# Kernel optimization log

Hardware: AMD Instinct MI355X
Metric: run time of the kernel (lower is better)

Reference implementation:

```python
import jax, jax.numpy as jnp
import numpy as np

N_NODES, N_EDGES, D_IN, D_HID, D_OUT = 100000, 3200000, 128, 64, 10


def _gcn_norm(src, dst, n):
    # symmetric normalization deg^{-1/2}[src] * deg^{-1/2}[dst]; edge weights = 1
    ones = jnp.ones(src.shape[0], jnp.float32)
    deg = jax.ops.segment_sum(ones, dst, num_segments=n)
    dinv = jnp.where(deg > 0, jax.lax.rsqrt(jnp.maximum(deg, 1.0)), 0.0)
    return dinv[src] * dinv[dst]


def _gcn_conv(x, W, b, src, dst, norm, n):
    h = x @ W                                   # [N, out]
    msg = norm[:, None] * jnp.take(h, src, axis=0)  # [E+N, out]
    return jax.ops.segment_sum(msg, dst, num_segments=n) + b


def setup_inputs() -> dict:
    key = jax.random.key(0)
    ks = jax.random.split(key, 8)
    x = jax.random.normal(ks[0], (N_NODES, D_IN), jnp.float32)
    edge_index = jax.random.randint(ks[1], (2, N_EDGES), 0, N_NODES, jnp.int32)
    def glorot(k, fan_in, fan_out):
        s = (6.0 / (fan_in + fan_out)) ** 0.5
        return jax.random.uniform(k, (fan_in, fan_out), jnp.float32, -s, s)
    return {
        "x": x,
        "edge_index": edge_index,
        "W1": glorot(ks[2], D_IN, D_HID), "b1": jnp.zeros((D_HID,), jnp.float32),
        "W2": glorot(ks[3], D_HID, D_HID), "b2": jnp.zeros((D_HID,), jnp.float32),
        "W3": glorot(ks[4], D_HID, D_OUT), "b3": jnp.zeros((D_OUT,), jnp.float32),
    }


def reference(x, edge_index, W1, b1, W2, b2, W3, b3):
    n = x.shape[0]
    loops = jnp.arange(n, dtype=edge_index.dtype)
    src = jnp.concatenate([edge_index[0], loops])  # add self-loops (PyG default)
    dst = jnp.concatenate([edge_index[1], loops])
    norm = _gcn_norm(src, dst, n)                  # identical for all 3 layers
    h = jax.nn.relu(_gcn_conv(x, W1, b1, src, dst, norm, n))
    h = jax.nn.relu(_gcn_conv(h, W2, b2, src, dst, norm, n))
    return _gcn_conv(h, W3, b3, src, dst, norm, n)
```

## Files before the change

### kernel.cpp

```cpp
#include <hip/hip_runtime.h>


constexpr int BK_SHIFT = 6;
constexpr int BK_NODES = 64;
constexpr int BK_CAP   = 2432;
constexpr int MAXNB    = 1568;

typedef __attribute__((ext_vector_type(8))) short short8_t;
typedef __attribute__((ext_vector_type(4))) float f32x4_t;

__device__ __forceinline__ unsigned short f2bf(float f) {
    unsigned u = __builtin_bit_cast(unsigned, f);
    u += 0x7FFF + ((u >> 16) & 1);
    return (unsigned short)(u >> 16);
}
__device__ __forceinline__ unsigned pack2(float lo, float hi) {
    return (unsigned)f2bf(lo) | ((unsigned)f2bf(hi) << 16);
}
__device__ __forceinline__ float bf_lo(unsigned d) {
    return __builtin_bit_cast(float, d << 16);
}
__device__ __forceinline__ float bf_hi(unsigned d) {
    return __builtin_bit_cast(float, d & 0xFFFF0000u);
}
__device__ __forceinline__ float bf1(unsigned short u) {
    return __builtin_bit_cast(float, (unsigned)u << 16);
}

__global__ void k_partition(const int* __restrict__ src, const int* __restrict__ dst,
                            int E, int nb, int* __restrict__ cursor,
                            unsigned* __restrict__ inter) {
    __shared__ int lcount[MAXNB];
    __shared__ int gbase[MAXNB];
    int t = threadIdx.x;
    int base = blockIdx.x * 16384;
    for (int i = t; i < MAXNB; i += 512) lcount[i] = 0;
    __syncthreads();
    int sv[32], dvv[32];
#pragma unroll
    for (int j = 0; j < 32; j++) {
        int idx = base + j * 512 + t;
        if (idx < E) {
            sv[j] = src[idx]; dvv[j] = dst[idx];
            atomicAdd(&lcount[dvv[j] >> BK_SHIFT], 1);
        } else dvv[j] = -1;
    }
    __syncthreads();
    for (int i = t; i < nb; i += 512) {
        int c = lcount[i]; int g = 0;
        if (c) g = atomicAdd(&cursor[i], c);
        gbase[i] = g; lcount[i] = 0;
    }
    __syncthreads();
#pragma unroll
    for (int j = 0; j < 32; j++) {
        if (dvv[j] >= 0) {
            int b = dvv[j] >> BK_SHIFT;
            int r = gbase[b] + atomicAdd(&lcount[b], 1);
            if (r < BK_CAP)
                inter[(size_t)b * BK_CAP + r] =
                    (unsigned)sv[j] | ((unsigned)(dvv[j] & (BK_NODES - 1)) << 20);
        }
    }
}

__global__ void k_dinvb(const unsigned* __restrict__ inter, const int* __restrict__ cursor,
                        float* __restrict__ dinv, int N) {
    __shared__ int hist[BK_NODES];
    int t = threadIdx.x, b = blockIdx.x;
    if (t < BK_NODES) hist[t] = 0;
    __syncthreads();
    int cnt = min(cursor[b], BK_CAP);
    const unsigned* ip = inter + (size_t)b * BK_CAP;
    for (int i = t; i < cnt; i += 256) atomicAdd(&hist[ip[i] >> 20], 1);
    __syncthreads();
    if (t < BK_NODES) {
        int d = b * BK_NODES + t;
        if (d < N) dinv[d] = rsqrtf((float)(hist[t] + 1));
    }
}

template <int K, bool IN_F32>
__global__ __launch_bounds__(256) void k_gemmMF(const void* __restrict__ Xv,
                           const float* __restrict__ W,
                           const float* __restrict__ dinv,
                           unsigned short* __restrict__ Y, int n) {
    constexpr int KP = K + 8;
    __shared__ unsigned short Al[64 * KP];
    __shared__ unsigned short Bl[64 * KP];
    int t = threadIdx.x;
    int nb = blockIdx.x * 64;
    if (IN_F32) {
        const float* X = (const float*)Xv;
        for (int i = t * 4; i < 64 * K; i += 1024) {
            int r = i / K, c = i % K;
            int node = nb + r;
            float4 v = {0.f, 0.f, 0.f, 0.f};
            if (node < n) v = *reinterpret_cast<const float4*>(X + (size_t)node * K + c);
            uint2 pk = {pack2(v.x, v.y), pack2(v.z, v.w)};
            *reinterpret_cast<uint2*>(&Al[r * KP + c]) = pk;
        }
    } else {
        const unsigned short* X = (const unsigned short*)Xv;
        for (int i = t * 4; i < 64 * K; i += 1024) {
            int r = i / K, c = i % K;
            int node = nb + r;
            uint2 pk = {0u, 0u};
            if (node < n) pk = *reinterpret_cast<const uint2*>(X + (size_t)node * K + c);
            *reinterpret_cast<uint2*>(&Al[r * KP + c]) = pk;
        }
    }
    {
        int c = t & 63, kb = t >> 6;
        for (int k = kb; k < K; k += 4)
            Bl[c * KP + k] = f2bf(W[k * 64 + c]);
    }
    __syncthreads();
    int w = t >> 6, lane = t & 63;
    int ml = lane & 15, kg = lane >> 4;
    f32x4_t acc[4] = {{0,0,0,0},{0,0,0,0},{0,0,0,0},{0,0,0,0}};
    for (int ks = 0; ks < K / 32; ks++) {
        int ko = ks * 32 + kg * 8;
        short8_t a = *reinterpret_cast<const short8_t*>(&Al[(16 * w + ml) * KP + ko]);
#pragma unroll
        for (int c = 0; c < 4; c++) {
            short8_t b = *reinterpret_cast<const short8_t*>(&Bl[(16 * c + ml) * KP + ko]);
            acc[c] = __builtin_amdgcn_mfma_f32_16x16x32_bf16(a, b, acc[c], 0, 0, 0);
        }
    }
#pragma unroll
    for (int r = 0; r < 4; r++) {
        int grow = nb + 16 * w + kg * 4 + r;
        if (grow < n) {
            float dv = dinv[grow];
#pragma unroll
            for (int c = 0; c < 4; c++)
                Y[(size_t)grow * 64 + 16 * c + ml] = f2bf(dv * acc[c][r]);
        }
    }
}

__global__ void k_gemm10(const float* __restrict__ X, const float* __restrict__ W,
                         const float* __restrict__ dinv, unsigned short* __restrict__ Y, int n) {
    __shared__ float ws[64 * 10];
    __shared__ float xs[16 * 64];
    int t = threadIdx.x;
    for (int i = t; i < 640; i += 256) ws[i] = W[i];
    int nb = blockIdx.x * 16;
    for (int i = t; i < 16 * 64; i += 256) {
        int r = i >> 6, c = i & 63;
        int node = nb + r;
        xs[i] = (node < n) ? X[(size_t)node * 64 + c] : 0.f;
    }
    __syncthreads();
    int ns = t >> 4, c = t & 15;
    if (c < 10) {
        float acc = 0.f;
        for (int k = 0; k < 64; k++) acc += xs[ns * 64 + k] * ws[k * 10 + c];
        int node = nb + ns;
        if (node < n) Y[(size_t)node * 10 + c] = f2bf(dinv[node] * acc);
    }
}

template <int OBF>
__global__ __launch_bounds__(512) void k_agg64(const unsigned short* __restrict__ H,
                        const unsigned* __restrict__ inter, const int* __restrict__ cursor,
                        const float* __restrict__ bias, void* __restrict__ outv,
                        int N, int relu) {
    __shared__ unsigned raw[BK_CAP];
    __shared__ unsigned srt[BK_CAP];
    __shared__ int hist[BK_NODES];
    __shared__ int offs[BK_NODES + 1];
    __shared__ int cur[BK_NODES];
    int t = threadIdx.x, b = blockIdx.x;
    if (t < BK_NODES) hist[t] = 0;
    __syncthreads();
    int cnt = min(cursor[b], BK_CAP);
    const unsigned* ip = inter + (size_t)b * BK_CAP;
    for (int i = t; i < cnt; i += 512) {
        unsigned r = ip[i];
        raw[i] = r;
        atomicAdd(&hist[r >> 20], 1);
    }
    __syncthreads();
    if (t < BK_NODES) {
        int v = hist[t];
        int inc = v;
#pragma unroll
        for (int d = 1; d < 64; d <<= 1) {
            int o = __shfl_up(inc, d);
            if (t >= d) inc += o;
        }
        offs[t + 1] = inc;
        if (t == 0) offs[0] = 0;
        cur[t] = inc - v;
    }
    __syncthreads();
    for (int i = t; i < cnt; i += 512) {
        unsigned r = raw[i];
        int pos = atomicAdd(&cur[r >> 20], 1);
        srt[pos] = r & 0xFFFFFu;
    }
    __syncthreads();
    int wv = t >> 6, lane = t & 63;
    int esub = lane >> 3, cg = lane & 7;
    const unsigned short* Hc = H + (cg << 3);
    for (int nd = wv; nd < BK_NODES; nd += 8) {
        int d = b * BK_NODES + nd;
        if (d >= N) break;
        int o0 = offs[nd], o1 = offs[nd + 1];
        float a0 = 0.f, a1 = 0.f, a2 = 0.f, a3 = 0.f;
        float a4 = 0.f, a5 = 0.f, a6 = 0.f, a7 = 0.f;
        int e = o0 + esub;
        for (; e + 8 < o1; e += 16) {
            int s0 = srt[e], s1 = srt[e + 8];
            const uint4 v0 = *reinterpret_cast<const uint4*>(Hc + ((size_t)s0 << 6));
            const uint4 v1 = *reinterpret_cast<const uint4*>(Hc + ((size_t)s1 << 6));
            a0 += bf_lo(v0.x); a1 += bf_hi(v0.x); a2 += bf_lo(v0.y); a3 += bf_hi(v0.y);
            a4 += bf_lo(v0.z); a5 += bf_hi(v0.z); a6 += bf_lo(v0.w); a7 += bf_hi(v0.w);
            a0 += bf_lo(v1.x); a1 += bf_hi(v1.x); a2 += bf_lo(v1.y); a3 += bf_hi(v1.y);
            a4 += bf_lo(v1.z); a5 += bf_hi(v1.z); a6 += bf_lo(v1.w); a7 += bf_hi(v1.w);
        }
        for (; e < o1; e += 8) {
            int s0 = srt[e];
            const uint4 v0 = *reinterpret_cast<const uint4*>(Hc + ((size_t)s0 << 6));
            a0 += bf_lo(v0.x); a1 += bf_hi(v0.x); a2 += bf_lo(v0.y); a3 += bf_hi(v0.y);
            a4 += bf_lo(v0.z); a5 += bf_hi(v0.z); a6 += bf_lo(v0.w); a7 += bf_hi(v0.w);
        }
#pragma unroll
        for (int m = 8; m <= 32; m <<= 1) {
            a0 += __shfl_xor(a0, m); a1 += __shfl_xor(a1, m);
            a2 += __shfl_xor(a2, m); a3 += __shfl_xor(a3, m);
            a4 += __shfl_xor(a4, m); a5 += __shfl_xor(a5, m);
            a6 += __shfl_xor(a6, m); a7 += __shfl_xor(a7, m);
        }
        if (esub == 0) {
            float dv = rsqrtf((float)(hist[nd] + 1));
            const uint4 sv = *reinterpret_cast<const uint4*>(Hc + ((size_t)d << 6));
            float s[8] = {bf_lo(sv.x), bf_hi(sv.x), bf_lo(sv.y), bf_hi(sv.y),
                          bf_lo(sv.z), bf_hi(sv.z), bf_lo(sv.w), bf_hi(sv.w)};
            float acc[8] = {a0, a1, a2, a3, a4, a5, a6, a7};
            const float* bp = bias + cg * 8;
            float o[8];
#pragma unroll
            for (int j = 0; j < 8; j++) {
                float val = dv * (acc[j] + s[j]) + bp[j];
                if (relu) val = fmaxf(val, 0.f);
                o[j] = val;
            }
            if (OBF) {
                unsigned short* op = (unsigned short*)outv + (size_t)d * 64 + cg * 8;
                uint4 pk = {pack2(o[0], o[1]), pack2(o[2], o[3]),
                            pack2(o[4], o[5]), pack2(o[6], o[7])};
                *reinterpret_cast<uint4*>(op) = pk;
            } else {
                float* op = (float*)outv + (size_t)d * 64 + cg * 8;
                float4 r0 = {o[0], o[1], o[2], o[3]}, r1 = {o[4], o[5], o[6], o[7]};
                *reinterpret_cast<float4*>(op)     = r0;
                *reinterpret_cast<float4*>(op + 4) = r1;
            }
        }
    }
}

__global__ __launch_bounds__(512) void k_agg10(const unsigned short* __restrict__ H,
                        const unsigned* __restrict__ inter, const int* __restrict__ cursor,
                        const float* __restrict__ b3, float* __restrict__ out, int N) {
    __shared__ unsigned raw[BK_CAP];
    __shared__ unsigned srt[BK_CAP];
    __shared__ int hist[BK_NODES];
    __shared__ int offs[BK_NODES + 1];
    __shared__ int cur[BK_NODES];
    int t = threadIdx.x, b = blockIdx.x;
    if (t < BK_NODES) hist[t] = 0;
    __syncthreads();
    int cnt = min(cursor[b], BK_CAP);
    const unsigned* ip = inter + (size_t)b * BK_CAP;
    for (int i = t; i < cnt; i += 512) {
        unsigned r = ip[i];
        raw[i] = r;
        atomicAdd(&hist[r >> 20], 1);
    }
    __syncthreads();
    if (t < BK_NODES) {
        int v = hist[t];
        int inc = v;
#pragma unroll
        for (int d = 1; d < 64; d <<= 1) {
            int o = __shfl_up(inc, d);
            if (t >= d) inc += o;
        }
        offs[t + 1] = inc;
        if (t == 0) offs[0] = 0;
        cur[t] = inc - v;
    }
    __syncthreads();
    for (int i = t; i < cnt; i += 512) {
        unsigned r = raw[i];
        int pos = atomicAdd(&cur[r >> 20], 1);
        srt[pos] = r & 0xFFFFFu;
    }
    __syncthreads();
    int wv = t >> 6, lane = t & 63;
    int esub = lane >> 4, c = lane & 15;
    for (int nd = wv; nd < BK_NODES; nd += 8) {
        int d = b * BK_NODES + nd;
        if (d >= N) break;
        int o0 = offs[nd], o1 = offs[nd + 1];
        float acc = 0.f;
        if (c < 10) {
            int e = o0 + esub;
            for (; e + 4 < o1; e += 8) {
                int s0 = srt[e], s1 = srt[e + 4];
                acc += bf1(H[(size_t)s0 * 10 + c]) + bf1(H[(size_t)s1 * 10 + c]);
            }
            if (e < o1) acc += bf1(H[(size_t)srt[e] * 10 + c]);
        }
        acc += __shfl_xor(acc, 16);
        acc += __shfl_xor(acc, 32);
        if (esub == 0 && c < 10) {
            float dv = rsqrtf((float)(hist[nd] + 1));
            out[(size_t)d * 10 + c] = dv * (acc + bf1(H[(size_t)d * 10 + c])) + b3[c];
        }
    }
}

extern "C" void kernel_launch(void* const* d_in, const int* in_sizes, int n_in,
                              void* d_out, int out_size, void* d_ws, size_t ws_size,
                              hipStream_t stream) {
    const float* x  = (const float*)d_in[0];
    const int*   ei = (const int*)d_in[1];
    const float* W1 = (const float*)d_in[2];
    const float* b1 = (const float*)d_in[3];
    const float* W2 = (const float*)d_in[4];
    const float* b2 = (const float*)d_in[5];
    const float* W3 = (const float*)d_in[6];
    const float* b3 = (const float*)d_in[7];

    int N = in_sizes[0] / 128;
    int E = in_sizes[1] / 2;
    const int* esrc = ei;
    const int* edst = ei + E;
    int nb = (N + BK_NODES - 1) >> BK_SHIFT;

    char* p = (char*)d_ws;
    auto carve = [&](size_t bytes) -> void* {
        void* r = p;
        p += (bytes + 255) & ~(size_t)255;
        return r;
    };
    int*      cursor = (int*)carve((size_t)MAXNB * 4);
    unsigned* inter  = (unsigned*)carve((size_t)nb * BK_CAP * 4);
    float*    dinv   = (float*)carve((size_t)N * 4);
    unsigned short* Hs = (unsigned short*)carve((size_t)N * 64 * 2);
    unsigned short* Gb = (unsigned short*)carve((size_t)N * 64 * 2);
    float*    Gf     = (float*)carve((size_t)N * 64 * 4);
    unsigned short* Hs10 = (unsigned short*)carve((size_t)N * 10 * 2);
    (void)ws_size; (void)n_in; (void)out_size;

    hipMemsetAsync(cursor, 0, (size_t)nb * 4, stream);
    k_partition<<<(E + 16383) / 16384, 512, 0, stream>>>(esrc, edst, E, nb, cursor, inter);
    k_dinvb<<<nb, 256, 0, stream>>>(inter, cursor, dinv, N);

    k_gemmMF<128, true><<<(N + 63) / 64, 256, 0, stream>>>(x, W1, dinv, Hs, N);
    k_agg64<1><<<nb, 512, 0, stream>>>(Hs, inter, cursor, b1, Gb, N, 1);
    k_gemmMF<64, false><<<(N + 63) / 64, 256, 0, stream>>>(Gb, W2, dinv, Hs, N);
    k_agg64<0><<<nb, 512, 0, stream>>>(Hs, inter, cursor, b2, Gf, N, 1);
    k_gemm10<<<(N + 15) / 16, 256, 0, stream>>>(Gf, W3, dinv, Hs10, N);
    k_agg10<<<nb, 512, 0, stream>>>(Hs10, inter, cursor, b3, (float*)d_out, N);
}
```

Baseline: 246.0 us.

## Presort bucket edges once and split 64-wide aggregation into feature quarters

```diff
diff --git a/kernel.cpp b/kernel.cpp
--- a/kernel.cpp
+++ b/kernel.cpp
@@ -64,20 +64,50 @@
     }
 }
 
-__global__ void k_dinvb(const unsigned* __restrict__ inter, const int* __restrict__ cursor,
+__global__ __launch_bounds__(512) void k_sort(const unsigned* __restrict__ inter,
+                        const int* __restrict__ cursor,
+                        unsigned* __restrict__ srt_g, int* __restrict__ offs_g,
                         float* __restrict__ dinv, int N) {
+    __shared__ unsigned raw[BK_CAP];
+    __shared__ unsigned srt[BK_CAP];
     __shared__ int hist[BK_NODES];
+    __shared__ int offs[BK_NODES + 1];
+    __shared__ int cur[BK_NODES];
     int t = threadIdx.x, b = blockIdx.x;
     if (t < BK_NODES) hist[t] = 0;
     __syncthreads();
     int cnt = min(cursor[b], BK_CAP);
     const unsigned* ip = inter + (size_t)b * BK_CAP;
-    for (int i = t; i < cnt; i += 256) atomicAdd(&hist[ip[i] >> 20], 1);
+    for (int i = t; i < cnt; i += 512) {
+        unsigned r = ip[i];
+        raw[i] = r;
+        atomicAdd(&hist[r >> 20], 1);
+    }
     __syncthreads();
     if (t < BK_NODES) {
+        int v = hist[t];
+        int inc = v;
+#pragma unroll
+        for (int d = 1; d < 64; d <<= 1) {
+            int o = __shfl_up(inc, d);
+            if (t >= d) inc += o;
+        }
+        offs[t + 1] = inc;
+        if (t == 0) offs[0] = 0;
+        cur[t] = inc - v;
         int d = b * BK_NODES + t;
         if (d < N) dinv[d] = rsqrtf((float)(hist[t] + 1));
     }
+    __syncthreads();
+    for (int i = t; i < cnt; i += 512) {
+        unsigned r = raw[i];
+        int pos = atomicAdd(&cur[r >> 20], 1);
+        srt[pos] = r & 0xFFFFFu;
+    }
+    __syncthreads();
+    unsigned* sg = srt_g + (size_t)b * BK_CAP;
+    for (int i = t; i < cnt; i += 512) sg[i] = srt[i];
+    if (t < BK_NODES + 1) offs_g[b * (BK_NODES + 1) + t] = offs[t];
 }
 
 template <int K, bool IN_F32>
@@ -135,7 +165,7 @@
             float dv = dinv[grow];
 #pragma unroll
             for (int c = 0; c < 4; c++)
-                Y[(size_t)grow * 64 + 16 * c + ml] = f2bf(dv * acc[c][r]);
+                Y[((size_t)c * n + grow) * 16 + ml] = f2bf(dv * acc[c][r]);
         }
     }
 }
@@ -163,153 +193,97 @@
 }
 
 template <int OBF>
-__global__ __launch_bounds__(512) void k_agg64(const unsigned short* __restrict__ H,
-                        const unsigned* __restrict__ inter, const int* __restrict__ cursor,
-                        const float* __restrict__ bias, void* __restrict__ outv,
-                        int N, int relu) {
-    __shared__ unsigned raw[BK_CAP];
+__global__ __launch_bounds__(256) void k_agg64s(const unsigned short* __restrict__ Hs,
+                        const unsigned* __restrict__ srt_g, const int* __restrict__ offs_g,
+                        const float* __restrict__ dinv, const float* __restrict__ bias,
+                        void* __restrict__ outv, int N, int nb, int relu) {
     __shared__ unsigned srt[BK_CAP];
-    __shared__ int hist[BK_NODES];
     __shared__ int offs[BK_NODES + 1];
-    __shared__ int cur[BK_NODES];
-    int t = threadIdx.x, b = blockIdx.x;
-    if (t < BK_NODES) hist[t] = 0;
-    __syncthreads();
-    int cnt = min(cursor[b], BK_CAP);
-    const unsigned* ip = inter + (size_t)b * BK_CAP;
-    for (int i = t; i < cnt; i += 512) {
-        unsigned r = ip[i];
-        raw[i] = r;
-        atomicAdd(&hist[r >> 20], 1);
-    }
-    __syncthreads();
-    if (t < BK_NODES) {
-        int v = hist[t];
-        int inc = v;
-#pragma unroll
-        for (int d = 1; d < 64; d <<= 1) {
-            int o = __shfl_up(inc, d);
-            if (t >= d) inc += o;
-        }
-        offs[t + 1] = inc;
-        if (t == 0) offs[0] = 0;
-        cur[t] = inc - v;
-    }
-    __syncthreads();
-    for (int i = t; i < cnt; i += 512) {
-        unsigned r = raw[i];
-        int pos = atomicAdd(&cur[r >> 20], 1);
-        srt[pos] = r & 0xFFFFFu;
-    }
-    __syncthreads();
+    int t = threadIdx.x;
+    int x = blockIdx.x & 7;
+    int q = x >> 1;
+    int b = (blockIdx.x >> 3) * 2 + (x & 1);
+    if (b >= nb) return;
+    if (t < BK_NODES + 1) offs[t] = offs_g[b * (BK_NODES + 1) + t];
+    __syncthreads();
+    int cnt = offs[BK_NODES];
+    const unsigned* sg = srt_g + (size_t)b * BK_CAP;
+    for (int i = t; i < cnt; i += 256) srt[i] = sg[i];
+    __syncthreads();
+    const unsigned short* Hq = Hs + (size_t)q * N * 16;
+    const float* bq = bias + q * 16;
     int wv = t >> 6, lane = t & 63;
-    int esub = lane >> 3, cg = lane & 7;
-    const unsigned short* Hc = H + (cg << 3);
-    for (int nd = wv; nd < BK_NODES; nd += 8) {
+    int es = lane >> 2, cg = lane & 3;
+    for (int nd = wv; nd < BK_NODES; nd += 4) {
         int d = b * BK_NODES + nd;
         if (d >= N) break;
         int o0 = offs[nd], o1 = offs[nd + 1];
         float a0 = 0.f, a1 = 0.f, a2 = 0.f, a3 = 0.f;
-        float a4 = 0.f, a5 = 0.f, a6 = 0.f, a7 = 0.f;
-        int e = o0 + esub;
-        for (; e + 8 < o1; e += 16) {
-            int s0 = srt[e], s1 = srt[e + 8];
-            const uint4 v0 = *reinterpret_cast<const uint4*>(Hc + ((size_t)s0 << 6));
-            const uint4 v1 = *reinterpret_cast<const uint4*>(Hc + ((size_t)s1 << 6));
-            a0 += bf_lo(v0.x); a1 += bf_hi(v0.x); a2 += bf_lo(v0.y); a3 += bf_hi(v0.y);
-            a4 += bf_lo(v0.z); a5 += bf_hi(v0.z); a6 += bf_lo(v0.w); a7 += bf_hi(v0.w);
-            a0 += bf_lo(v1.x); a1 += bf_hi(v1.x); a2 += bf_lo(v1.y); a3 += bf_hi(v1.y);
-            a4 += bf_lo(v1.z); a5 += bf_hi(v1.z); a6 += bf_lo(v1.w); a7 += bf_hi(v1.w);
-        }
-        for (; e < o1; e += 8) {
+        int e = o0 + es;
+        for (; e + 16 < o1; e += 32) {
+            int s0 = srt[e], s1 = srt[e + 16];
+            const uint2 v0 = *reinterpret_cast<const uint2*>(Hq + (size_t)s0 * 16 + cg * 4);
+            const uint2 v1 = *reinterpret_cast<const uint2*>(Hq + (size_t)s1 * 16 + cg * 4);
+            a0 += bf_lo(v0.x) + bf_lo(v1.x); a1 += bf_hi(v0.x) + bf_hi(v1.x);
+            a2 += bf_lo(v0.y) + bf_lo(v1.y); a3 += bf_hi(v0.y) + bf_hi(v1.y);
+        }
+        for (; e < o1; e += 16) {
             int s0 = srt[e];
-            const uint4 v0 = *reinterpret_cast<const uint4*>(Hc + ((size_t)s0 << 6));
-            a0 += bf_lo(v0.x); a1 += bf_hi(v0.x); a2 += bf_lo(v0.y); a3 += bf_hi(v0.y);
-            a4 += bf_lo(v0.z); a5 += bf_hi(v0.z); a6 += bf_lo(v0.w); a7 += bf_hi(v0.w);
-        }
-#pragma unroll
-        for (int m = 8; m <= 32; m <<= 1) {
+            const uint2 v0 = *reinterpret_cast<const uint2*>(Hq + (size_t)s0 * 16 + cg * 4);
+            a0 += bf_lo(v0.x); a1 += bf_hi(v0.x);
+            a2 += bf_lo(v0.y); a3 += bf_hi(v0.y);
+        }
+#pragma unroll
+        for (int m = 4; m <= 32; m <<= 1) {
             a0 += __shfl_xor(a0, m); a1 += __shfl_xor(a1, m);
             a2 += __shfl_xor(a2, m); a3 += __shfl_xor(a3, m);
-            a4 += __shfl_xor(a4, m); a5 += __shfl_xor(a5, m);
-            a6 += __shfl_xor(a6, m); a7 += __shfl_xor(a7, m);
-        }
-        if (esub == 0) {
-            float dv = rsqrtf((float)(hist[nd] + 1));
-            const uint4 sv = *reinterpret_cast<const uint4*>(Hc + ((size_t)d << 6));
-            float s[8] = {bf_lo(sv.x), bf_hi(sv.x), bf_lo(sv.y), bf_hi(sv.y),
-                          bf_lo(sv.z), bf_hi(sv.z), bf_lo(sv.w), bf_hi(sv.w)};
-            float acc[8] = {a0, a1, a2, a3, a4, a5, a6, a7};
-            const float* bp = bias + cg * 8;
-            float o[8];
-#pragma unroll
-            for (int j = 0; j < 8; j++) {
-                float val = dv * (acc[j] + s[j]) + bp[j];
+        }
+        if (es == 0) {
+            float dv = dinv[d];
+            const uint2 sv = *reinterpret_cast<const uint2*>(Hq + (size_t)d * 16 + cg * 4);
+            float o[4] = {bf_lo(sv.x), bf_hi(sv.x), bf_lo(sv.y), bf_hi(sv.y)};
+            float ac[4] = {a0, a1, a2, a3};
+#pragma unroll
+            for (int j = 0; j < 4; j++) {
+                float val = dv * (ac[j] + o[j]) + bq[cg * 4 + j];
                 if (relu) val = fmaxf(val, 0.f);
                 o[j] = val;
             }
             if (OBF) {
-                unsigned short* op = (unsigned short*)outv + (size_t)d * 64 + cg * 8;
-                uint4 pk = {pack2(o[0], o[1]), pack2(o[2], o[3]),
-                            pack2(o[4], o[5]), pack2(o[6], o[7])};
-                *reinterpret_cast<uint4*>(op) = pk;
+                unsigned short* op = (unsigned short*)outv + (size_t)d * 64 + q * 16 + cg * 4;
+                uint2 pk = {pack2(o[0], o[1]), pack2(o[2], o[3])};
+                *reinterpret_cast<uint2*>(op) = pk;
             } else {
-                float* op = (float*)outv + (size_t)d * 64 + cg * 8;
-                float4 r0 = {o[0], o[1], o[2], o[3]}, r1 = {o[4], o[5], o[6], o[7]};
-                *reinterpret_cast<float4*>(op)     = r0;
-                *reinterpret_cast<float4*>(op + 4) = r1;
+                float* op = (float*)outv + (size_t)d * 64 + q * 16 + cg * 4;
+                float4 r0 = {o[0], o[1], o[2], o[3]};
+                *reinterpret_cast<float4*>(op) = r0;
             }
         }
     }
 }
 
-__global__ __launch_bounds__(512) void k_agg10(const unsigned short* __restrict__ H,
-                        const unsigned* __restrict__ inter, const int* __restrict__ cursor,
-                        const float* __restrict__ b3, float* __restrict__ out, int N) {
-    __shared__ unsigned raw[BK_CAP];
+__global__ __launch_bounds__(512) void k_agg10s(const unsigned short* __restrict__ H,
+                        const unsigned* __restrict__ srt_g, const int* __restrict__ offs_g,
+                        const float* __restrict__ dinv, const float* __restrict__ b3,
+                        float* __restrict__ out, int N) {
     __shared__ unsigned srt[BK_CAP];
-    __shared__ int hist[BK_NODES];
     __shared__ int offs[BK_NODES + 1];
-    __shared__ int cur[BK_NODES];
     int t = threadIdx.x, b = blockIdx.x;
-    if (t < BK_NODES) hist[t] = 0;
-    __syncthreads();
-    int cnt = min(cursor[b], BK_CAP);
-    const unsigned* ip = inter + (size_t)b * BK_CAP;
-    for (int i = t; i < cnt; i += 512) {
-        unsigned r = ip[i];
-        raw[i] = r;
-        atomicAdd(&hist[r >> 20], 1);
-    }
-    __syncthreads();
-    if (t < BK_NODES) {
-        int v = hist[t];
-        int inc = v;
-#pragma unroll
-        for (int d = 1; d < 64; d <<= 1) {
-            int o = __shfl_up(inc, d);
-            if (t >= d) inc += o;
-        }
-        offs[t + 1] = inc;
-        if (t == 0) offs[0] = 0;
-        cur[t] = inc - v;
-    }
-    __syncthreads();
-    for (int i = t; i < cnt; i += 512) {
-        unsigned r = raw[i];
-        int pos = atomicAdd(&cur[r >> 20], 1);
-        srt[pos] = r & 0xFFFFFu;
-    }
+    if (t < BK_NODES + 1) offs[t] = offs_g[b * (BK_NODES + 1) + t];
+    __syncthreads();
+    int cnt = offs[BK_NODES];
+    const unsigned* sg = srt_g + (size_t)b * BK_CAP;
+    for (int i = t; i < cnt; i += 512) srt[i] = sg[i];
     __syncthreads();
     int wv = t >> 6, lane = t & 63;
-    int esub = lane >> 4, c = lane & 15;
+    int es = lane >> 4, c = lane & 15;
     for (int nd = wv; nd < BK_NODES; nd += 8) {
         int d = b * BK_NODES + nd;
         if (d >= N) break;
         int o0 = offs[nd], o1 = offs[nd + 1];
         float acc = 0.f;
         if (c < 10) {
-            int e = o0 + esub;
+            int e = o0 + es;
             for (; e + 4 < o1; e += 8) {
                 int s0 = srt[e], s1 = srt[e + 4];
                 acc += bf1(H[(size_t)s0 * 10 + c]) + bf1(H[(size_t)s1 * 10 + c]);
@@ -318,8 +292,8 @@
         }
         acc += __shfl_xor(acc, 16);
         acc += __shfl_xor(acc, 32);
-        if (esub == 0 && c < 10) {
-            float dv = rsqrtf((float)(hist[nd] + 1));
+        if (es == 0 && c < 10) {
+            float dv = dinv[d];
             out[(size_t)d * 10 + c] = dv * (acc + bf1(H[(size_t)d * 10 + c])) + b3[c];
         }
     }
@@ -351,6 +325,8 @@
     };
     int*      cursor = (int*)carve((size_t)MAXNB * 4);
     unsigned* inter  = (unsigned*)carve((size_t)nb * BK_CAP * 4);
+    unsigned* srt_g  = (unsigned*)carve((size_t)nb * BK_CAP * 4);
+    int*      offs_g = (int*)carve((size_t)nb * (BK_NODES + 1) * 4);
     float*    dinv   = (float*)carve((size_t)N * 4);
     unsigned short* Hs = (unsigned short*)carve((size_t)N * 64 * 2);
     unsigned short* Gb = (unsigned short*)carve((size_t)N * 64 * 2);
@@ -358,14 +334,16 @@
     unsigned short* Hs10 = (unsigned short*)carve((size_t)N * 10 * 2);
     (void)ws_size; (void)n_in; (void)out_size;
 
+    int gridA = ((nb + 1) / 2) * 8;
+
     hipMemsetAsync(cursor, 0, (size_t)nb * 4, stream);
     k_partition<<<(E + 16383) / 16384, 512, 0, stream>>>(esrc, edst, E, nb, cursor, inter);
-    k_dinvb<<<nb, 256, 0, stream>>>(inter, cursor, dinv, N);
+    k_sort<<<nb, 512, 0, stream>>>(inter, cursor, srt_g, offs_g, dinv, N);
 
     k_gemmMF<128, true><<<(N + 63) / 64, 256, 0, stream>>>(x, W1, dinv, Hs, N);
-    k_agg64<1><<<nb, 512, 0, stream>>>(Hs, inter, cursor, b1, Gb, N, 1);
+    k_agg64s<1><<<gridA, 256, 0, stream>>>(Hs, srt_g, offs_g, dinv, b1, Gb, N, nb, 1);
     k_gemmMF<64, false><<<(N + 63) / 64, 256, 0, stream>>>(Gb, W2, dinv, Hs, N);
-    k_agg64<0><<<nb, 512, 0, stream>>>(Hs, inter, cursor, b2, Gf, N, 1);
+    k_agg64s<0><<<gridA, 256, 0, stream>>>(Hs, srt_g, offs_g, dinv, b2, Gf, N, nb, 1);
     k_gemm10<<<(N + 15) / 16, 256, 0, stream>>>(Gf, W3, dinv, Hs10, N);
-    k_agg10<<<nb, 512, 0, stream>>>(Hs10, inter, cursor, b3, (float*)d_out, N);
-}
+    k_agg10s<<<nb, 512, 0, stream>>>(Hs10, srt_g, offs_g, dinv, b3, (float*)d_out, N);
+}
```

New measurement: 333.7 us. 35.7% more time.
